# Kernel tuning notes

Hardware: AMD Instinct MI355X
Metric: run time of the kernel (lower is better)

The kernel has to match this reference:

```python
import jax, jax.numpy as jnp
import numpy as np

HIDDEN = 4096
NUM_Q = 32
NUM_KV = 8
HEAD_DIM = 128
EPS = 1e-6
ROPE_THETA = 1e6


def _rmsnorm(x, w):
    # x: [..., HEAD_DIM]
    var = jnp.mean(x * x, axis=-1, keepdims=True)
    return x * jax.lax.rsqrt(var + EPS) * w


def _rope(x, positions):
    # x: [n_tok, H, HEAD_DIM], rotate-half convention
    half = HEAD_DIM // 2
    inv_freq = 1.0 / (ROPE_THETA ** (jnp.arange(0, half, dtype=jnp.float32) / half))
    freqs = positions.astype(jnp.float32)[:, None] * inv_freq  # [n_tok, half]
    cos = jnp.concatenate([jnp.cos(freqs), jnp.cos(freqs)], axis=-1)[:, None, :]
    sin = jnp.concatenate([jnp.sin(freqs), jnp.sin(freqs)], axis=-1)[:, None, :]
    x1, x2 = x[..., :half], x[..., half:]
    rot = jnp.concatenate([-x2, x1], axis=-1)
    return x * cos + rot * sin


def setup_inputs() -> dict:
    key = jax.random.key(0)
    ks = jax.random.split(key, 7)
    n_tok = 2048
    s = 0.02
    return {
        "hidden": jax.random.normal(ks[0], (n_tok, HIDDEN), dtype=jnp.float32),
        "positions": jnp.arange(n_tok, dtype=jnp.int32),
        "Wq": jax.random.normal(ks[1], (HIDDEN, NUM_Q * HEAD_DIM), dtype=jnp.float32) * s,
        "Wk": jax.random.normal(ks[2], (HIDDEN, NUM_KV * HEAD_DIM), dtype=jnp.float32) * s,
        "Wv": jax.random.normal(ks[3], (HIDDEN, NUM_KV * HEAD_DIM), dtype=jnp.float32) * s,
        "Wo": jax.random.normal(ks[4], (NUM_Q * HEAD_DIM, HIDDEN), dtype=jnp.float32) * s,
        "q_norm_w": jnp.ones((HEAD_DIM,), dtype=jnp.float32),
        "k_norm_w": jnp.ones((HEAD_DIM,), dtype=jnp.float32),
    }


def reference(hidden, positions, Wq, Wk, Wv, Wo, q_norm_w, k_norm_w):
    n_tok = hidden.shape[0]
    group = NUM_Q // NUM_KV

    q = (hidden @ Wq).reshape(n_tok, NUM_Q, HEAD_DIM)
    k = (hidden @ Wk).reshape(n_tok, NUM_KV, HEAD_DIM)
    v = (hidden @ Wv).reshape(n_tok, NUM_KV, HEAD_DIM)

    q = _rmsnorm(q, q_norm_w)
    k = _rmsnorm(k, k_norm_w)
    q = _rope(q, positions)
    k = _rope(k, positions)

    # GQA: group q heads [n_tok, NUM_KV, group, HEAD_DIM]
    qg = q.reshape(n_tok, NUM_KV, group, HEAD_DIM)
    scale = 1.0 / np.sqrt(HEAD_DIM)
    scores = jnp.einsum("qhgd,khd->hgqk", qg, k) * scale  # [NUM_KV, group, n_tok, n_tok]
    causal = jnp.tril(jnp.ones((n_tok, n_tok), dtype=bool))
    scores = jnp.where(causal, scores, jnp.finfo(scores.dtype).min)
    probs = jax.nn.softmax(scores, axis=-1)
    out = jnp.einsum("hgqk,khd->qhgd", probs, v)  # [n_tok, NUM_KV, group, HEAD_DIM]
    out = out.reshape(n_tok, NUM_Q * HEAD_DIM)
    return out @ Wo
```

## Files before the change

### kernel.cpp

```cpp
#include <hip/hip_runtime.h>
#include <stdint.h>

typedef unsigned short u16;
typedef __bf16 bf16_t;
typedef bf16_t bf16x8 __attribute__((ext_vector_type(8)));
typedef float f32x4 __attribute__((ext_vector_type(4)));
typedef float f32x16 __attribute__((ext_vector_type(16)));
typedef u16 u16x4 __attribute__((ext_vector_type(4)));
typedef u16 u16x8 __attribute__((ext_vector_type(8)));
typedef uint32_t u32x4 __attribute__((ext_vector_type(4)));
typedef int i32x2 __attribute__((ext_vector_type(2)));

#define HIDDEN 4096
#define NTOK 2048
#define NQ 32
#define NKV 8
#define HD 128
#define QKV_N 6144

#define AS1 __attribute__((address_space(1)))
#define AS3 __attribute__((address_space(3)))

__device__ __forceinline__ u16 f2bf(float f) {
  union { float f; uint32_t u; } v; v.f = f;
  uint32_t u = v.u;
  return (u16)((u + 0x7fffu + ((u >> 16) & 1u)) >> 16);
}

__global__ void cvt_hidden(const float* __restrict__ src, u16* __restrict__ dst, int n4) {
  int i = blockIdx.x * blockDim.x + threadIdx.x;
  if (i >= n4) return;
  float4 v = ((const float4*)src)[i];
  u16x4 o;
  o[0] = f2bf(v.x); o[1] = f2bf(v.y); o[2] = f2bf(v.z); o[3] = f2bf(v.w);
  ((u16x4*)dst)[i] = o;
}

__global__ void transpose_cvt(const float* __restrict__ src, u16* __restrict__ dst,
                              int R, int C) {
  __shared__ float tile[64][65];
  int tx = threadIdx.x & 63;
  int ty = threadIdx.x >> 6;
  int r0 = blockIdx.y * 64, c0 = blockIdx.x * 64;
  for (int i = 0; i < 16; i++) {
    int r = ty + i * 4;
    tile[r][tx] = src[(size_t)(r0 + r) * C + c0 + tx];
  }
  __syncthreads();
  for (int i = 0; i < 16; i++) {
    int c = ty + i * 4;
    dst[(size_t)(c0 + c) * R + r0 + tx] = f2bf(tile[tx][c]);
  }
}

#define BARRIER() do { asm volatile("" ::: "memory"); __builtin_amdgcn_s_barrier(); asm volatile("" ::: "memory"); } while (0)
#define WAIT_LGKM0() asm volatile("s_waitcnt lgkmcnt(0)" ::: "memory")
#define WAIT_VM4() asm volatile("s_waitcnt vmcnt(4)" ::: "memory")
#define WAIT_VM0() asm volatile("s_waitcnt vmcnt(0)" ::: "memory")

#define STAGE_A(buf, half, t) do { \
  __builtin_amdgcn_global_load_lds((AS1 void*)(void*)(gA + (size_t)((half) * 128) * K + (t) * 64), \
      (AS3 void*)(void*)(&sA[buf][((half) * 128) * 64 + lds0]), 16, 0, 0); \
  __builtin_amdgcn_global_load_lds((AS1 void*)(void*)(gA + (size_t)((half) * 128 + 64) * K + (t) * 64), \
      (AS3 void*)(void*)(&sA[buf][((half) * 128 + 64) * 64 + lds0]), 16, 0, 0); \
} while (0)

#define STAGE_B(buf, half, t) do { \
  __builtin_amdgcn_global_load_lds((AS1 void*)(void*)(gB + (size_t)((half) * 128) * K + (t) * 64), \
      (AS3 void*)(void*)(&sB[buf][((half) * 128) * 64 + lds0]), 16, 0, 0); \
  __builtin_amdgcn_global_load_lds((AS1 void*)(void*)(gB + (size_t)((half) * 128 + 64) * K + (t) * 64), \
      (AS3 void*)(void*)(&sB[buf][((half) * 128 + 64) * 64 + lds0]), 16, 0, 0); \
} while (0)

#define RD_A(buf, mh, dst) do { \
  _Pragma("unroll") for (int m_ = 0; m_ < 4; m_++) \
  _Pragma("unroll") for (int s_ = 0; s_ < 2; s_++) \
    dst[m_][s_] = *(const bf16x8*)(const void*)(&sA[buf][(wy * 128 + ((mh) * 4 + m_) * 16 + l16) * 64 + ((s_ * 4 + quad) ^ swz) * 8]); \
} while (0)

#define RD_B(buf, nh, dst) do { \
  _Pragma("unroll") for (int n_ = 0; n_ < 2; n_++) \
  _Pragma("unroll") for (int s_ = 0; s_ < 2; s_++) \
    dst[n_][s_] = *(const bf16x8*)(const void*)(&sB[buf][(wx * 64 + ((nh) * 2 + n_) * 16 + l16) * 64 + ((s_ * 4 + quad) ^ swz) * 8]); \
} while (0)

#define MFMA16(mh, nh, a_, b_) do { \
  __builtin_amdgcn_s_setprio(1); \
  _Pragma("unroll") for (int s_ = 0; s_ < 2; s_++) \
  _Pragma("unroll") for (int m_ = 0; m_ < 4; m_++) \
  _Pragma("unroll") for (int n_ = 0; n_ < 2; n_++) \
    acc[(mh) * 4 + m_][(nh) * 2 + n_] = __builtin_amdgcn_mfma_f32_16x16x32_bf16( \
        a_[m_][s_], b_[n_][s_], acc[(mh) * 4 + m_][(nh) * 2 + n_], 0, 0, 0); \
  __builtin_amdgcn_s_setprio(0); \
} while (0)

__global__ __launch_bounds__(512, 2) void gemm256(const u16* __restrict__ A,
                                                  const u16* __restrict__ B,
                                                  float* __restrict__ C,
                                                  int M, int N, int K) {
  __shared__ u16 sA[2][256 * 64];
  __shared__ u16 sB[2][256 * 64];
  const int tid = threadIdx.x;
  const int wave = tid >> 6, lane = tid & 63;
  const int quad = lane >> 4, l16 = lane & 15;
  const int wy = wave >> 2, wx = wave & 3;
  const int row0 = blockIdx.y * 256, col0 = blockIdx.x * 256;
  f32x4 acc[8][4] = {};
  const int srow = tid >> 3, schunk = tid & 7;
  const int gchunk = schunk ^ (srow & 7);
  const u16* gA = A + (size_t)(row0 + srow) * K + gchunk * 8;
  const u16* gB = B + (size_t)(col0 + srow) * K + gchunk * 8;
  const int lds0 = srow * 64 + schunk * 8;
  const int swz = l16 & 7;

  STAGE_B(0, 0, 0); STAGE_B(0, 1, 0); STAGE_A(0, 0, 0); STAGE_A(0, 1, 0);
  STAGE_B(1, 0, 1); STAGE_B(1, 1, 1);
  WAIT_VM4();
  BARRIER();

  const int nIter = (K >> 6) >> 1;
  for (int i = 0; i < nIter; i++) {
    const int tb = 2 * i + 1, t2 = 2 * i + 2, t3 = 2 * i + 3;
    const bool more = (i + 1 < nIter);
    bf16x8 a0[4][2], a1[4][2], b0[2][2], b1[2][2];
    RD_A(0, 0, a0); RD_B(0, 0, b0);
    STAGE_A(1, 0, tb);
    BARRIER(); WAIT_LGKM0(); MFMA16(0, 0, a0, b0); BARRIER();
    RD_B(0, 1, b1);
    STAGE_A(1, 1, tb);
    BARRIER(); WAIT_LGKM0(); MFMA16(0, 1, a0, b1); BARRIER();
    RD_A(0, 1, a1);
    if (more) STAGE_B(0, 0, t2);
    BARRIER(); WAIT_LGKM0(); MFMA16(1, 1, a1, b1); BARRIER();
    if (more) { STAGE_B(0, 1, t2); WAIT_VM4(); } else { WAIT_VM0(); }
    BARRIER(); MFMA16(1, 0, a1, b0); BARRIER();
    RD_A(1, 0, a0); RD_B(1, 0, b0);
    if (more) STAGE_A(0, 0, t2);
    BARRIER(); WAIT_LGKM0(); MFMA16(0, 0, a0, b0); BARRIER();
    RD_B(1, 1, b1);
    if (more) STAGE_A(0, 1, t2);
    BARRIER(); WAIT_LGKM0(); MFMA16(0, 1, a0, b1); BARRIER();
    RD_A(1, 1, a1);
    if (more) STAGE_B(1, 0, t3);
    BARRIER(); WAIT_LGKM0(); MFMA16(1, 1, a1, b1); BARRIER();
    if (more) { STAGE_B(1, 1, t3); WAIT_VM4(); }
    BARRIER(); MFMA16(1, 0, a1, b0); BARRIER();
  }

#pragma unroll
  for (int mi = 0; mi < 8; mi++)
#pragma unroll
    for (int ni = 0; ni < 4; ni++) {
      int row = row0 + wy * 128 + mi * 16 + quad * 4;
      int col = col0 + wx * 64 + ni * 16 + l16;
      float* cp = C + (size_t)row * N + col;
#pragma unroll
      for (int r = 0; r < 4; r++) cp[(size_t)r * N] = acc[mi][ni][r];
    }
}

__global__ void normrope(const float* __restrict__ qkv, const int* __restrict__ pos,
                         const float* __restrict__ qw, const float* __restrict__ kw,
                         u16* __restrict__ Qo, u16* __restrict__ Ko) {
  const int hh = blockIdx.x;
  const int t = blockIdx.y * 4 + (threadIdx.x >> 6);
  const int lane = threadIdx.x & 63;
  const bool isQ = hh < NQ;
  const int col = isQ ? hh * HD : HIDDEN + (hh - NQ) * HD;
  const float* src = qkv + (size_t)t * QKV_N + col;
  float x1 = src[lane], x2 = src[lane + 64];
  float ss = x1 * x1 + x2 * x2;
  for (int m = 1; m < 64; m <<= 1) ss += __shfl_xor(ss, m);
  float inv = rsqrtf(ss * (1.0f / 128.0f) + 1e-6f);
  const float* w = isQ ? qw : kw;
  x1 *= inv * w[lane];
  x2 *= inv * w[lane + 64];
  float p = (float)pos[t];
  float freq = expf((float)lane * -0.2158673525f);
  float a = p * freq;
  float sn = sinf(a), cs = cosf(a);
  float o1 = x1 * cs - x2 * sn;
  float o2 = x2 * cs + x1 * sn;
  const float osc = isQ ? 0.08838834764831845f : 1.0f;
  u16* dst = isQ ? (Qo + (size_t)t * (NQ * HD) + hh * HD)
                 : (Ko + (size_t)t * (NKV * HD) + (hh - NQ) * HD);
  dst[lane] = f2bf(o1 * osc);
  dst[lane + 64] = f2bf(o2 * osc);
}

__global__ void vtrans(const float* __restrict__ qkv, u16* __restrict__ vT) {
  __shared__ float s[128][65];
  int tb = blockIdx.x;
  int vh = blockIdx.y;
  int tid = threadIdx.x;
  for (int i = 0; i < 32; i++) {
    int e = i * 256 + tid;
    int tl = e >> 7;
    int d = e & 127;
    s[d][tl] = qkv[(size_t)(tb * 64 + tl) * QKV_N + 5120 + vh * 128 + d];
  }
  __syncthreads();
  for (int i = 0; i < 32; i++) {
    int e = i * 256 + tid;
    int d = e >> 6;
    int tl = e & 63;
    vT[(size_t)vh * (HD * NTOK) + (size_t)d * NTOK + tb * 64 + tl] = f2bf(s[d][tl]);
  }
}

__global__ __launch_bounds__(512, 2) void flash3(const u16* __restrict__ Q,
                                                 const u16* __restrict__ K,
                                                 const u16* __restrict__ V,
                                                 u16* __restrict__ O) {
  __shared__ u16 sK[64 * 136];
  __shared__ u16 sV[128 * 72];
  const int lid = blockIdx.x;
  const int kvh = lid & 7;
  const int head = kvh * 4 + ((lid >> 3) & 3);
  const int p = lid >> 5;
  const int tid = threadIdx.x;
  const int wave = tid >> 6, lane = tid & 63;
  const int l32 = lane & 31, h = lane >> 5;
  const int tileq = (wave < 4) ? p : (15 - p);
  const int qrow0 = tileq * 128 + (wave & 3) * 32;
  const u16* Vh = V + (size_t)kvh * (HD * NTOK);

  bf16x8 qf[8];
  const u16* qbase = Q + (size_t)(qrow0 + l32) * (NQ * HD) + head * HD + h * 8;
#pragma unroll
  for (int ks = 0; ks < 8; ks++)
    qf[ks] = *(const bf16x8*)(const void*)(qbase + ks * 16);

  f32x16 accO[4] = {};
  float l_loc = 0.f;
  const int nU = 32 - 2 * p;
  const int rk0 = tid >> 4, ck0 = tid & 15;
  const int rv0 = tid >> 3, cv0 = tid & 7;
  const u16* Kr = K + (size_t)kvh * HD + ck0 * 8;
  const u16* Vr = Vh + (size_t)rv0 * NTOK + cv0 * 8;
  const u16* Vr2 = Vh + (size_t)(rv0 + 64) * NTOK + cv0 * 8;

  u16x8 k0 = *(const u16x8*)(const void*)(Kr + (size_t)rk0 * (NKV * HD));
  u16x8 k1 = *(const u16x8*)(const void*)(Kr + (size_t)(rk0 + 32) * (NKV * HD));
  u16x8 v0 = *(const u16x8*)(const void*)(Vr);
  u16x8 v1 = *(const u16x8*)(const void*)(Vr2);

  for (int kb = 0; kb < nU; kb++) {
    __syncthreads();
    *(u16x8*)(void*)(sK + rk0 * 136 + ck0 * 8) = k0;
    *(u16x8*)(void*)(sK + (rk0 + 32) * 136 + ck0 * 8) = k1;
    *(u16x8*)(void*)(sV + rv0 * 72 + cv0 * 8) = v0;
    *(u16x8*)(void*)(sV + (rv0 + 64) * 72 + cv0 * 8) = v1;
    __syncthreads();
    if (kb + 1 < nU) {
      const size_t koff = (size_t)((kb + 1) * 64) * (NKV * HD);
      k0 = *(const u16x8*)(const void*)(Kr + koff + (size_t)rk0 * (NKV * HD));
      k1 = *(const u16x8*)(const void*)(Kr + koff + (size_t)(rk0 + 32) * (NKV * HD));
      v0 = *(const u16x8*)(const void*)(Vr + (kb + 1) * 64);
      v1 = *(const u16x8*)(const void*)(Vr2 + (kb + 1) * 64);
    }
    const int t0 = kb * 64;
    if (t0 > qrow0 + 31) continue;
    const bool act1 = (t0 + 32 <= qrow0 + 31);

    f32x16 s0 = {}, s1 = {};
#pragma unroll
    for (int ks = 0; ks < 8; ks++) {
      bf16x8 kf0 = *(const bf16x8*)(const void*)(sK + l32 * 136 + ks * 16 + h * 8);
      s0 = __builtin_amdgcn_mfma_f32_32x32x16_bf16(kf0, qf[ks], s0, 0, 0, 0);
    }
    if (act1) {
#pragma unroll
      for (int ks = 0; ks < 8; ks++) {
        bf16x8 kf1 = *(const bf16x8*)(const void*)(sK + (32 + l32) * 136 + ks * 16 + h * 8);
        s1 = __builtin_amdgcn_mfma_f32_32x32x16_bf16(kf1, qf[ks], s1, 0, 0, 0);
      }
    }

    auto process = [&](const f32x16& sv_, int tb) {
      float pr[16];
      const int tbase = t0 + tb * 32;
      const int qg = qrow0 + l32;
      if (tbase + 31 <= qrow0) {
#pragma unroll
        for (int r = 0; r < 16; r++) { float e = __expf(sv_[r]); pr[r] = e; l_loc += e; }
      } else {
#pragma unroll
        for (int r = 0; r < 16; r++) {
          const int tok = tbase + (r & 3) + 8 * (r >> 2) + 4 * h;
          float e = (tok <= qg) ? __expf(sv_[r]) : 0.f;
          pr[r] = e; l_loc += e;
        }
      }
#pragma unroll
      for (int u = 0; u < 2; u++) {
        uint32_t A0, A1, B0, B1;
        asm("v_cvt_pk_bf16_f32 %0, %1, %2" : "=v"(A0) : "v"(pr[u * 8 + 0]), "v"(pr[u * 8 + 1]));
        asm("v_cvt_pk_bf16_f32 %0, %1, %2" : "=v"(A1) : "v"(pr[u * 8 + 2]), "v"(pr[u * 8 + 3]));
        asm("v_cvt_pk_bf16_f32 %0, %1, %2" : "=v"(B0) : "v"(pr[u * 8 + 4]), "v"(pr[u * 8 + 5]));
        asm("v_cvt_pk_bf16_f32 %0, %1, %2" : "=v"(B1) : "v"(pr[u * 8 + 6]), "v"(pr[u * 8 + 7]));
#if __has_builtin(__builtin_amdgcn_permlane32_swap)
        i32x2 r02 = __builtin_amdgcn_permlane32_swap((int)A0, (int)B0, false, false);
        i32x2 r13 = __builtin_amdgcn_permlane32_swap((int)A1, (int)B1, false, false);
        const uint32_t w0 = (uint32_t)r02.x, w2 = (uint32_t)r02.y;
        const uint32_t w1 = (uint32_t)r13.x, w3 = (uint32_t)r13.y;
#else
        const uint32_t A0x = (uint32_t)__shfl_xor((int)A0, 32);
        const uint32_t A1x = (uint32_t)__shfl_xor((int)A1, 32);
        const uint32_t B0x = (uint32_t)__shfl_xor((int)B0, 32);
        const uint32_t B1x = (uint32_t)__shfl_xor((int)B1, 32);
        const uint32_t w0 = h ? B0x : A0;
        const uint32_t w1 = h ? B1x : A1;
        const uint32_t w2 = h ? B0 : A0x;
        const uint32_t w3 = h ? B1 : A1x;
#endif
        union { u32x4 w; bf16x8 v; } pf;
        pf.w = (u32x4){w0, w1, w2, w3};
#pragma unroll
        for (int db = 0; db < 4; db++) {
          bf16x8 vf = *(const bf16x8*)(const void*)(sV + (db * 32 + l32) * 72 + tb * 32 + u * 16 + h * 8);
          accO[db] = __builtin_amdgcn_mfma_f32_32x32x16_bf16(vf, pf.v, accO[db], 0, 0, 0);
        }
      }
    };
    process(s0, 0);
    if (act1) process(s1, 1);
  }

  l_loc += __shfl_xor(l_loc, 32);
  const float inv = 1.0f / l_loc;
  u16* ob = O + (size_t)(qrow0 + l32) * (NQ * HD) + head * HD;
#pragma unroll
  for (int db = 0; db < 4; db++)
#pragma unroll
    for (int g = 0; g < 4; g++) {
      u16x4 o4;
#pragma unroll
      for (int j = 0; j < 4; j++) o4[j] = f2bf(accO[db][4 * g + j] * inv);
      *(u16x4*)(void*)(ob + db * 32 + g * 8 + h * 4) = o4;
    }
}

extern "C" void kernel_launch(void* const* d_in, const int* in_sizes, int n_in,
                              void* d_out, int out_size, void* d_ws, size_t ws_size,
                              hipStream_t stream) {
  const float* hidden = (const float*)d_in[0];
  const int* positions = (const int*)d_in[1];
  const float* Wq = (const float*)d_in[2];
  const float* Wk = (const float*)d_in[3];
  const float* Wv = (const float*)d_in[4];
  const float* Wo = (const float*)d_in[5];
  const float* qw = (const float*)d_in[6];
  const float* kw = (const float*)d_in[7];
  char* ws = (char*)d_ws;
  u16* hid_bf  = (u16*)(ws);
  u16* WqkvT   = (u16*)(ws + 16777216);
  u16* WoT     = (u16*)(ws + 67108864);
  float* qkvf  = (float*)(ws + 100663296);
  u16* Qn      = (u16*)(ws + 150994944);
  u16* Kn      = (u16*)(ws + 167772160);
  u16* Vt      = (u16*)(ws + 171966464);
  u16* AO      = (u16*)(ws + 176160768);
  float* outp  = (float*)d_out;

  cvt_hidden<<<NTOK * HIDDEN / 4 / 256, 256, 0, stream>>>(hidden, hid_bf, NTOK * HIDDEN / 4);
  transpose_cvt<<<dim3(64, 64), 256, 0, stream>>>(Wq, WqkvT, 4096, 4096);
  transpose_cvt<<<dim3(16, 64), 256, 0, stream>>>(Wk, WqkvT + (size_t)4096 * 4096, 4096, 1024);
  transpose_cvt<<<dim3(16, 64), 256, 0, stream>>>(Wv, WqkvT + (size_t)5120 * 4096, 4096, 1024);
  transpose_cvt<<<dim3(64, 64), 256, 0, stream>>>(Wo, WoT, 4096, 4096);
  gemm256<<<dim3(24, 8), 512, 0, stream>>>(hid_bf, WqkvT, qkvf, 2048, 6144, 4096);
  normrope<<<dim3(40, 512), 256, 0, stream>>>(qkvf, positions, qw, kw, Qn, Kn);
  vtrans<<<dim3(32, 8), 256, 0, stream>>>(qkvf, Vt);
  flash3<<<dim3(256), 512, 0, stream>>>(Qn, Kn, Vt, AO);
  gemm256<<<dim3(16, 8), 512, 0, stream>>>(AO, WoT, outp, 2048, 4096, 4096);
}
```

Baseline: 551.8 us.

## Software-pipeline LDS fragment reads with MFMA in bf16 GEMM main loop

```diff
diff --git a/kernel.cpp b/kernel.cpp
--- a/kernel.cpp
+++ b/kernel.cpp
@@ -54,7 +54,6 @@
 }
 
 #define BARRIER() do { asm volatile("" ::: "memory"); __builtin_amdgcn_s_barrier(); asm volatile("" ::: "memory"); } while (0)
-#define WAIT_LGKM0() asm volatile("s_waitcnt lgkmcnt(0)" ::: "memory")
 #define WAIT_VM4() asm volatile("s_waitcnt vmcnt(4)" ::: "memory")
 #define WAIT_VM0() asm volatile("s_waitcnt vmcnt(0)" ::: "memory")
 
@@ -118,33 +117,51 @@
   WAIT_VM4();
   BARRIER();
 
+  bf16x8 a0[4][2], a1[4][2], b0[2][2], b1[2][2];
+  RD_A(0, 0, a0); RD_B(0, 0, b0);
+
   const int nIter = (K >> 6) >> 1;
   for (int i = 0; i < nIter; i++) {
     const int tb = 2 * i + 1, t2 = 2 * i + 2, t3 = 2 * i + 3;
     const bool more = (i + 1 < nIter);
-    bf16x8 a0[4][2], a1[4][2], b0[2][2], b1[2][2];
-    RD_A(0, 0, a0); RD_B(0, 0, b0);
     STAGE_A(1, 0, tb);
-    BARRIER(); WAIT_LGKM0(); MFMA16(0, 0, a0, b0); BARRIER();
+    BARRIER();
     RD_B(0, 1, b1);
+    MFMA16(0, 0, a0, b0);
+    BARRIER();
     STAGE_A(1, 1, tb);
-    BARRIER(); WAIT_LGKM0(); MFMA16(0, 1, a0, b1); BARRIER();
+    BARRIER();
     RD_A(0, 1, a1);
+    MFMA16(0, 1, a0, b1);
+    BARRIER();
     if (more) STAGE_B(0, 0, t2);
-    BARRIER(); WAIT_LGKM0(); MFMA16(1, 1, a1, b1); BARRIER();
+    BARRIER();
+    MFMA16(1, 1, a1, b1);
+    BARRIER();
     if (more) { STAGE_B(0, 1, t2); WAIT_VM4(); } else { WAIT_VM0(); }
-    BARRIER(); MFMA16(1, 0, a1, b0); BARRIER();
-    RD_A(1, 0, a0); RD_B(1, 0, b0);
+    BARRIER();
+    RD_A(1, 0, a0); RD_B(1, 1, b1);
+    MFMA16(1, 0, a1, b0);
+    BARRIER();
     if (more) STAGE_A(0, 0, t2);
-    BARRIER(); WAIT_LGKM0(); MFMA16(0, 0, a0, b0); BARRIER();
-    RD_B(1, 1, b1);
+    BARRIER();
+    RD_B(1, 0, b0);
+    MFMA16(0, 1, a0, b1);
+    BARRIER();
     if (more) STAGE_A(0, 1, t2);
-    BARRIER(); WAIT_LGKM0(); MFMA16(0, 1, a0, b1); BARRIER();
+    BARRIER();
     RD_A(1, 1, a1);
+    MFMA16(0, 0, a0, b0);
+    BARRIER();
     if (more) STAGE_B(1, 0, t3);
-    BARRIER(); WAIT_LGKM0(); MFMA16(1, 1, a1, b1); BARRIER();
+    BARRIER();
+    MFMA16(1, 0, a1, b0);
+    BARRIER();
     if (more) { STAGE_B(1, 1, t3); WAIT_VM4(); }
-    BARRIER(); MFMA16(1, 0, a1, b0); BARRIER();
+    BARRIER();
+    if (more) { RD_A(0, 0, a0); RD_B(0, 0, b0); }
+    MFMA16(1, 1, a1, b1);
+    BARRIER();
   }
 
 #pragma unroll
```

After: 677.2 us. 1.23x slower.
